# Optimization experiments

Measured on AMD Instinct MI355X. Metric: run time of the kernel, lower is better.

Reference implementation:

```python
import jax, jax.numpy as jnp
import numpy as np

V, E, H, ENC = 10000, 512, 512, 2048
B, T, P = 64, 64, 196


def setup_inputs() -> dict:
    key = jax.random.key(0)
    ks = jax.random.split(key, 12)
    s = 0.02
    return {
        "encoder_out": jax.random.normal(ks[0], (B, P, ENC), jnp.float32),
        "targets": jax.random.randint(ks[1], (B, T), 0, V),
        "embedding": jax.random.normal(ks[2], (V, E), jnp.float32) * s,
        "W_ih": jax.random.normal(ks[3], (4 * H, E), jnp.float32) * s,
        "W_hh": jax.random.normal(ks[4], (4 * H, H), jnp.float32) * s,
        "b_ih": jnp.zeros((4 * H,), jnp.float32),
        "b_hh": jnp.zeros((4 * H,), jnp.float32),
        "Wh": jax.random.normal(ks[5], (H, ENC), jnp.float32) * s,
        "bh": jnp.zeros((H,), jnp.float32),
        "Wc": jax.random.normal(ks[6], (H, ENC), jnp.float32) * s,
        "bc": jnp.zeros((H,), jnp.float32),
        "Wout": jax.random.normal(ks[7], (V, H), jnp.float32) * s,
        "bout": jnp.zeros((V,), jnp.float32),
    }


def reference(encoder_out, targets, embedding, W_ih, W_hh, b_ih, b_hh, Wh, bh, Wc, bc, Wout, bout):
    # init hidden state from mean-pooled encoder features
    mean_enc = encoder_out.mean(axis=1)                      # [B, ENC]
    h0 = jnp.tanh(mean_enc @ Wh.T + bh)                      # [B, H]
    c0 = jnp.tanh(mean_enc @ Wc.T + bc)                      # [B, H]

    Bsz, Tlen = targets.shape
    # teacher forcing (ratio=1.0): input at step t is targets[:, t-1]
    emb = embedding[targets[:, :-1]]                         # [B, T-1, E]
    # precompute input-dependent gate pre-activations (dropout = eval identity)
    xg = jnp.einsum('bte,ge->btg', emb, W_ih) + b_ih + b_hh  # [B, T-1, 4H]

    def step(carry, x):
        h, c = carry
        gates = x + h @ W_hh.T                               # [B, 4H]
        i, f, g, o = jnp.split(gates, 4, axis=-1)
        i = jax.nn.sigmoid(i)
        f = jax.nn.sigmoid(f)
        g = jnp.tanh(g)
        o = jax.nn.sigmoid(o)
        c = f * c + i * g
        h = o * jnp.tanh(c)
        out = h @ Wout.T + bout                              # [B, V]
        return (h, c), out

    _, outs = jax.lax.scan(step, (h0, c0), jnp.swapaxes(xg, 0, 1))
    outs = jnp.swapaxes(outs, 0, 1)                          # [B, T-1, V]
    zeros0 = jnp.zeros((Bsz, 1, outs.shape[-1]), outs.dtype)  # step 0 untouched
    return jnp.concatenate([zeros0, outs], axis=1)           # [B, T, V]
```

## Files before the change

### kernel.cpp

```cpp
#include <hip/hip_runtime.h>

typedef __bf16 bf16x8 __attribute__((ext_vector_type(8)));
typedef float f32x4 __attribute__((ext_vector_type(4)));

static __device__ __forceinline__ unsigned short f2bf(float f) {
    unsigned u = __builtin_bit_cast(unsigned, f);
    unsigned r = u + 0x7fffu + ((u >> 16) & 1u);
    return (unsigned short)(r >> 16);
}

#define GLD_LDS16(g, l) __builtin_amdgcn_global_load_lds( \
    (const __attribute__((address_space(1))) unsigned int*)(const void*)(g), \
    (__attribute__((address_space(3))) unsigned int*)(void*)(l), 16, 0, 0)

__global__ __launch_bounds__(256) void k_prep(
    const float* Wih, const float* Whh, const float* Wh, const float* Wc,
    const float* Wout, const float* emb, const int* targets,
    unsigned short* Wih_b, unsigned short* Whh_b, unsigned short* Wh_b,
    unsigned short* Wc_b, unsigned short* Wout_b, unsigned short* Aemb,
    float* out, int* ctrs, float* ps)
{
    const long N0 = 1048576, N1 = 1048576, N2 = 1048576, N3 = 1048576;
    const long N4 = 5120000, N5 = 2064384, N6 = 640000, N7 = 256, N8 = 65536;
    const long total = N0 + N1 + N2 + N3 + N4 + N5 + N6 + N7 + N8;
    const long stride = (long)gridDim.x * blockDim.x;
    for (long i = (long)blockIdx.x * blockDim.x + threadIdx.x; i < total; i += stride) {
        long j = i;
        if (j < N0) { Wih_b[j] = f2bf(Wih[j]); continue; } j -= N0;
        if (j < N1) { Whh_b[j] = f2bf(Whh[j]); continue; } j -= N1;
        if (j < N2) { Wh_b[j]  = f2bf(Wh[j]);  continue; } j -= N2;
        if (j < N3) { Wc_b[j]  = f2bf(Wc[j]);  continue; } j -= N3;
        if (j < N4) { Wout_b[j] = f2bf(Wout[j]); continue; } j -= N4;
        if (j < N5) {
            long m = j >> 9; int k = (int)(j & 511);
            int b = (int)(m / 63), t = (int)(m - (long)b * 63);
            int row = targets[b * 64 + t];
            Aemb[j] = f2bf(emb[(long)row * 512 + k]);
            continue;
        } j -= N5;
        if (j < N6) {
            long b = j / 10000, v = j - b * 10000;
            out[b * 640000 + v] = 0.f;
            continue;
        } j -= N6;
        if (j < N7) { ctrs[j] = 0; continue; } j -= N7;
        ps[j] = 0.f;
    }
}

__global__ __launch_bounds__(128) void k_mean(const float* enc, unsigned short* mean_b)
{
    int b = blockIdx.y;
    int c = blockIdx.x * 128 + threadIdx.x;
    const float* base = enc + (long)b * 196 * 2048 + c;
    float s0 = 0.f, s1 = 0.f, s2 = 0.f, s3 = 0.f;
    for (int p = 0; p < 196; p += 4) {
        s0 += base[(long)(p + 0) * 2048];
        s1 += base[(long)(p + 1) * 2048];
        s2 += base[(long)(p + 2) * 2048];
        s3 += base[(long)(p + 3) * 2048];
    }
    mean_b[(long)b * 2048 + c] = f2bf((s0 + s1 + s2 + s3) * (1.f / 196.f));
}

__global__ __launch_bounds__(256) void k_h0c0(
    const unsigned short* A, const unsigned short* Whb, const unsigned short* Wcb,
    float* ps)
{
    __shared__ unsigned short As[64 * 40];
    __shared__ unsigned short Bs[64 * 40];
    const int tid = threadIdx.x;
    const int n0 = blockIdx.x * 64;
    const int kc = blockIdx.y * 16;
    const int w = tid >> 6, lane = tid & 63, quad = lane >> 4, l16 = lane & 15;
    const int r = tid >> 2, seg = tid & 3;
    f32x4 acc[4];
#pragma unroll
    for (int i = 0; i < 4; i++) acc[i] = (f32x4){0.f, 0.f, 0.f, 0.f};

    for (int kb = kc; kb < kc + 16; kb++) {
        int k0 = kb * 32;
        *(uint4*)&As[r * 40 + seg * 8] = *(const uint4*)&A[(long)r * 2048 + k0 + seg * 8];
        int ngr = n0 + r;
        const unsigned short* bsrc = (ngr < 512) ? (Whb + (long)ngr * 2048)
                                                 : (Wcb + (long)(ngr - 512) * 2048);
        *(uint4*)&Bs[r * 40 + seg * 8] = *(const uint4*)&bsrc[k0 + seg * 8];
        __syncthreads();
        bf16x8 bfr = *(const bf16x8*)&Bs[(16 * w + l16) * 40 + quad * 8];
#pragma unroll
        for (int mt = 0; mt < 4; mt++) {
            bf16x8 af = *(const bf16x8*)&As[(mt * 16 + l16) * 40 + quad * 8];
            acc[mt] = __builtin_amdgcn_mfma_f32_16x16x32_bf16(af, bfr, acc[mt], 0, 0, 0);
        }
        __syncthreads();
    }
    int ng = n0 + 16 * w + l16;
#pragma unroll
    for (int mt = 0; mt < 4; mt++) {
#pragma unroll
        for (int rr = 0; rr < 4; rr++) {
            int m = mt * 16 + quad * 4 + rr;
            atomicAdd(&ps[(long)m * 1024 + ng], acc[mt][rr]);
        }
    }
}

__global__ __launch_bounds__(256) void k_fin(
    const float* ps, const float* bh, const float* bc,
    unsigned short* Hbuf, float* c0buf)
{
    int i = blockIdx.x * 256 + threadIdx.x;
    int m = i >> 10, ng = i & 1023;
    int j = ng & 511;
    float bias = (ng < 512) ? bh[j] : bc[j];
    float v = tanhf(ps[i] + bias);
    if (ng < 512) Hbuf[(long)m * 512 + j] = f2bf(v);
    else          c0buf[(long)m * 512 + j] = v;
}

__global__ __launch_bounds__(256) void k_xg(
    const unsigned short* A, const unsigned short* Bw,
    const float* bih, const float* bhh, float* xg)
{
    __shared__ unsigned short As[64 * 40];
    __shared__ unsigned short Bs[64 * 40];
    const int tid = threadIdx.x;
    const int n0 = blockIdx.x * 64, m0 = blockIdx.y * 64;
    const int w = tid >> 6, lane = tid & 63, quad = lane >> 4, l16 = lane & 15;
    const int r = tid >> 2, seg = tid & 3;
    f32x4 acc[4];
#pragma unroll
    for (int i = 0; i < 4; i++) acc[i] = (f32x4){0.f, 0.f, 0.f, 0.f};

    for (int kb = 0; kb < 16; kb++) {
        int k0 = kb * 32;
        *(uint4*)&As[r * 40 + seg * 8] = *(const uint4*)&A[(long)(m0 + r) * 512 + k0 + seg * 8];
        *(uint4*)&Bs[r * 40 + seg * 8] = *(const uint4*)&Bw[(long)(n0 + r) * 512 + k0 + seg * 8];
        __syncthreads();
        bf16x8 bfr = *(const bf16x8*)&Bs[(16 * w + l16) * 40 + quad * 8];
#pragma unroll
        for (int mt = 0; mt < 4; mt++) {
            bf16x8 af = *(const bf16x8*)&As[(mt * 16 + l16) * 40 + quad * 8];
            acc[mt] = __builtin_amdgcn_mfma_f32_16x16x32_bf16(af, bfr, acc[mt], 0, 0, 0);
        }
        __syncthreads();
    }
    int ng = n0 + 16 * w + l16;
    float bias = bih[ng] + bhh[ng];
#pragma unroll
    for (int mt = 0; mt < 4; mt++) {
#pragma unroll
        for (int rr = 0; rr < 4; rr++) {
            int m = m0 + mt * 16 + quad * 4 + rr;
            xg[(long)m * 2048 + ng] = acc[mt][rr] + bias;
        }
    }
}

__global__ __launch_bounds__(256, 1) void k_scan(
    const unsigned short* Whh_b, const float* xg, const float* c0buf,
    unsigned short* Hbuf, int* ctrs)
{
    __shared__ unsigned short Wlds[128 * 520];
    __shared__ unsigned short hs[16 * 520];
    __shared__ float gs[16 * 133];
    const int tid = threadIdx.x;
    const int gid = blockIdx.x;
    const int b0 = (gid & 3) * 16;
    const int j0 = (gid >> 2) * 32;
    const int w = tid >> 6, lane = tid & 63, quad = lane >> 4, l16 = lane & 15;
    const int m = tid >> 4, u0 = (tid & 15) * 2;

    for (int nrel = w; nrel < 128; nrel += 4) {
        int q = nrel >> 5, u = nrel & 31;
        *(uint4*)&Wlds[nrel * 520 + lane * 8] =
            *(const uint4*)&Whh_b[(long)(q * 512 + j0 + u) * 512 + lane * 8];
    }
    float2 cr = *(const float2*)&c0buf[(long)(b0 + m) * 512 + j0 + u0];
    float c0v = cr.x, c1v = cr.y;
    int* ctr = ctrs + (gid & 3) * 64;
    __syncthreads();

    for (int s = 1; s < 64; s++) {
        const float* xb = xg + ((long)(b0 + m) * 63 + (s - 1)) * 2048 + j0 + u0;
        float2 xv0 = *(const float2*)(xb + 0);
        float2 xv1 = *(const float2*)(xb + 512);
        float2 xv2 = *(const float2*)(xb + 1024);
        float2 xv3 = *(const float2*)(xb + 1536);

        const unsigned* hsrc = (const unsigned*)(Hbuf + ((long)(s - 1) * 64 + b0) * 512);
        unsigned hv[16];
#pragma unroll
        for (int j = 0; j < 16; j++)
            hv[j] = __hip_atomic_load(hsrc + j * 256 + tid, __ATOMIC_RELAXED,
                                      __HIP_MEMORY_SCOPE_AGENT);
#pragma unroll
        for (int j = 0; j < 16; j++)
            *(unsigned*)&hs[j * 520 + tid * 2] = hv[j];
        __syncthreads();

        f32x4 acc0 = (f32x4){0.f, 0.f, 0.f, 0.f};
        f32x4 acc1 = (f32x4){0.f, 0.f, 0.f, 0.f};
#pragma unroll
        for (int kk = 0; kk < 16; kk++) {
            bf16x8 a  = *(const bf16x8*)&hs[l16 * 520 + kk * 32 + quad * 8];
            bf16x8 bA = *(const bf16x8*)&Wlds[(32 * w + l16) * 520 + kk * 32 + quad * 8];
            bf16x8 bB = *(const bf16x8*)&Wlds[(32 * w + 16 + l16) * 520 + kk * 32 + quad * 8];
            acc0 = __builtin_amdgcn_mfma_f32_16x16x32_bf16(a, bA, acc0, 0, 0, 0);
            acc1 = __builtin_amdgcn_mfma_f32_16x16x32_bf16(a, bB, acc1, 0, 0, 0);
        }
#pragma unroll
        for (int rr = 0; rr < 4; rr++) {
            gs[(quad * 4 + rr) * 133 + 32 * w + l16] = acc0[rr];
            gs[(quad * 4 + rr) * 133 + 32 * w + 16 + l16] = acc1[rr];
        }
        __syncthreads();

        float gi0 = gs[m * 133 + u0]          + xv0.x;
        float gi1 = gs[m * 133 + u0 + 1]      + xv0.y;
        float gf0 = gs[m * 133 + 32 + u0]     + xv1.x;
        float gf1 = gs[m * 133 + 33 + u0]     + xv1.y;
        float gg0 = gs[m * 133 + 64 + u0]     + xv2.x;
        float gg1 = gs[m * 133 + 65 + u0]     + xv2.y;
        float go0 = gs[m * 133 + 96 + u0]     + xv3.x;
        float go1 = gs[m * 133 + 97 + u0]     + xv3.y;
        float cn0 = (1.f / (1.f + __expf(-gf0))) * c0v + (1.f / (1.f + __expf(-gi0))) * tanhf(gg0);
        float cn1 = (1.f / (1.f + __expf(-gf1))) * c1v + (1.f / (1.f + __expf(-gi1))) * tanhf(gg1);
        c0v = cn0; c1v = cn1;
        float h0v = (1.f / (1.f + __expf(-go0))) * tanhf(cn0);
        float h1v = (1.f / (1.f + __expf(-go1))) * tanhf(cn1);
        unsigned hp = (unsigned)f2bf(h0v) | ((unsigned)f2bf(h1v) << 16);
        __hip_atomic_store((unsigned*)(Hbuf + ((long)s * 64 + b0 + m) * 512 + j0 + u0), hp,
                           __ATOMIC_RELAXED, __HIP_MEMORY_SCOPE_AGENT);

        if (s < 63) {
            __syncthreads();
            if (tid == 0) {
                __hip_atomic_fetch_add(ctr, 1, __ATOMIC_RELEASE, __HIP_MEMORY_SCOPE_AGENT);
                int target = s * 16;
                while (__hip_atomic_load(ctr, __ATOMIC_RELAXED, __HIP_MEMORY_SCOPE_AGENT) < target) {}
            }
            __syncthreads();
        }
    }
}

__global__ __launch_bounds__(256) void k_out(
    const unsigned short* A, const unsigned short* Wob, const float* bout, float* out)
{
    __shared__ unsigned short As[128 * 32];
    __shared__ unsigned short Bs[128 * 32];
    const int tid = threadIdx.x;
    const int n0 = blockIdx.x * 128, m0 = blockIdx.y * 128;
    const int w = tid >> 6, lane = tid & 63, quad = lane >> 4, l16 = lane & 15;
    const int wm = w >> 1, wn = w & 1;
    const int gr = lane >> 2, gc = (lane & 3) * 8;

    f32x4 acc[4][4];
#pragma unroll
    for (int i = 0; i < 4; i++)
#pragma unroll
        for (int j = 0; j < 4; j++) acc[i][j] = (f32x4){0.f, 0.f, 0.f, 0.f};

    for (int kb = 0; kb < 16; kb++) {
        int k0 = kb * 32;
#pragma unroll
        for (int p = 0; p < 2; p++) {
            int rowa = m0 + p * 64 + w * 16 + gr;
            GLD_LDS16(A + (long)rowa * 512 + k0 + gc, As + (p * 64 + w * 16) * 32);
            int rowb = n0 + p * 64 + w * 16 + gr;
            GLD_LDS16(Wob + (long)rowb * 512 + k0 + gc, Bs + (p * 64 + w * 16) * 32);
        }
        __syncthreads();
        bf16x8 af[4], bf[4];
#pragma unroll
        for (int mt = 0; mt < 4; mt++)
            af[mt] = *(const bf16x8*)&As[(wm * 64 + mt * 16 + l16) * 32 + quad * 8];
#pragma unroll
        for (int nt = 0; nt < 4; nt++)
            bf[nt] = *(const bf16x8*)&Bs[(wn * 64 + nt * 16 + l16) * 32 + quad * 8];
#pragma unroll
        for (int mt = 0; mt < 4; mt++)
#pragma unroll
            for (int nt = 0; nt < 4; nt++)
                acc[mt][nt] = __builtin_amdgcn_mfma_f32_16x16x32_bf16(af[mt], bf[nt], acc[mt][nt], 0, 0, 0);
        __syncthreads();
    }
#pragma unroll
    for (int nt = 0; nt < 4; nt++) {
        int n = n0 + wn * 64 + nt * 16 + l16;
        if (n >= 10000) continue;
        float bias = bout[n];
#pragma unroll
        for (int mt = 0; mt < 4; mt++) {
#pragma unroll
            for (int rr = 0; rr < 4; rr++) {
                int r = m0 + wm * 64 + mt * 16 + quad * 4 + rr;
                if (r < 4032) {
                    int s = (r >> 6) + 1, b = r & 63;
                    out[((long)b * 64 + s) * 10000 + n] = acc[mt][nt][rr] + bias;
                }
            }
        }
    }
}

extern "C" void kernel_launch(void* const* d_in, const int* in_sizes, int n_in,
                              void* d_out, int out_size, void* d_ws, size_t ws_size,
                              hipStream_t stream)
{
    const float* enc     = (const float*)d_in[0];
    const int*   targets = (const int*)d_in[1];
    const float* emb     = (const float*)d_in[2];
    const float* Wih     = (const float*)d_in[3];
    const float* Whh     = (const float*)d_in[4];
    const float* bih     = (const float*)d_in[5];
    const float* bhh     = (const float*)d_in[6];
    const float* Wh      = (const float*)d_in[7];
    const float* bh      = (const float*)d_in[8];
    const float* Wc      = (const float*)d_in[9];
    const float* bc      = (const float*)d_in[10];
    const float* Wout    = (const float*)d_in[11];
    const float* bout    = (const float*)d_in[12];
    float* out = (float*)d_out;

    char* ws = (char*)d_ws;
    size_t off = 0;
    auto alloc = [&](size_t bytes) {
        void* p = ws + off;
        off = (off + bytes + 255) & ~(size_t)255;
        return p;
    };
    unsigned short* mean_b = (unsigned short*)alloc((size_t)64 * 2048 * 2);
    unsigned short* Wih_b  = (unsigned short*)alloc((size_t)2048 * 512 * 2);
    unsigned short* Whh_b  = (unsigned short*)alloc((size_t)2048 * 512 * 2);
    unsigned short* Wh_b   = (unsigned short*)alloc((size_t)512 * 2048 * 2);
    unsigned short* Wc_b   = (unsigned short*)alloc((size_t)512 * 2048 * 2);
    unsigned short* Wout_b = (unsigned short*)alloc((size_t)10000 * 512 * 2);
    unsigned short* Aemb   = (unsigned short*)alloc((size_t)4032 * 512 * 2);
    float*          xg     = (float*)alloc((size_t)4032 * 2048 * 4);
    unsigned short* Hbuf   = (unsigned short*)alloc((size_t)64 * 64 * 512 * 2);
    float*          c0buf  = (float*)alloc((size_t)64 * 512 * 4);
    int*            ctrs   = (int*)alloc(256 * 4);
    float*          ps     = (float*)alloc((size_t)64 * 1024 * 4);

    k_prep<<<4096, 256, 0, stream>>>(Wih, Whh, Wh, Wc, Wout, emb, targets,
                                     Wih_b, Whh_b, Wh_b, Wc_b, Wout_b, Aemb, out, ctrs, ps);
    k_mean<<<dim3(16, 64), 128, 0, stream>>>(enc, mean_b);
    k_h0c0<<<dim3(16, 4), 256, 0, stream>>>(mean_b, Wh_b, Wc_b, ps);
    k_fin<<<256, 256, 0, stream>>>(ps, bh, bc, Hbuf, c0buf);
    k_xg<<<dim3(32, 63), 256, 0, stream>>>(Aemb, Wih_b, bih, bhh, xg);
    k_scan<<<64, 256, 0, stream>>>(Whh_b, xg, c0buf, Hbuf, ctrs);
    k_out<<<dim3(79, 32), 256, 0, stream>>>(Hbuf + 64 * 512, Wout_b, bout, out);
}
```

Baseline: 653.3 us.

## Vectorize prep, fold mean into prep, merge h0c0 and xg GEMMs, swizzle k_out tiles

The prep kernel is rewritten with block-range dispatch and 8-wide vectorized fp32-to-bf16 conversion, and it now also computes the encoder mean, which removes the separate k_mean launch. The h0/c0 GEMM and the xg GEMM are merged into one launch. The xg part switches to 128x128 tiles loaded with direct global-to-LDS loads, with buffers padded to cover the partial last tile. k_out now uses a 1D grid with a tile remapping meant to improve L2 reuse. Together these aim to cut launch overhead and memory inefficiency in the pre-scan stages, at the cost of more branchy dispatch code.

```diff
diff --git a/kernel.cpp b/kernel.cpp
--- a/kernel.cpp
+++ b/kernel.cpp
@@ -15,92 +15,176 @@
 
 __global__ __launch_bounds__(256) void k_prep(
     const float* Wih, const float* Whh, const float* Wh, const float* Wc,
-    const float* Wout, const float* emb, const int* targets,
+    const float* Wout, const float* emb, const int* targets, const float* enc,
     unsigned short* Wih_b, unsigned short* Whh_b, unsigned short* Wh_b,
     unsigned short* Wc_b, unsigned short* Wout_b, unsigned short* Aemb,
-    float* out, int* ctrs, float* ps)
-{
-    const long N0 = 1048576, N1 = 1048576, N2 = 1048576, N3 = 1048576;
-    const long N4 = 5120000, N5 = 2064384, N6 = 640000, N7 = 256, N8 = 65536;
-    const long total = N0 + N1 + N2 + N3 + N4 + N5 + N6 + N7 + N8;
-    const long stride = (long)gridDim.x * blockDim.x;
-    for (long i = (long)blockIdx.x * blockDim.x + threadIdx.x; i < total; i += stride) {
-        long j = i;
-        if (j < N0) { Wih_b[j] = f2bf(Wih[j]); continue; } j -= N0;
-        if (j < N1) { Whh_b[j] = f2bf(Whh[j]); continue; } j -= N1;
-        if (j < N2) { Wh_b[j]  = f2bf(Wh[j]);  continue; } j -= N2;
-        if (j < N3) { Wc_b[j]  = f2bf(Wc[j]);  continue; } j -= N3;
-        if (j < N4) { Wout_b[j] = f2bf(Wout[j]); continue; } j -= N4;
-        if (j < N5) {
-            long m = j >> 9; int k = (int)(j & 511);
-            int b = (int)(m / 63), t = (int)(m - (long)b * 63);
-            int row = targets[b * 64 + t];
-            Aemb[j] = f2bf(emb[(long)row * 512 + k]);
-            continue;
-        } j -= N5;
-        if (j < N6) {
-            long b = j / 10000, v = j - b * 10000;
-            out[b * 640000 + v] = 0.f;
-            continue;
-        } j -= N6;
-        if (j < N7) { ctrs[j] = 0; continue; } j -= N7;
-        ps[j] = 0.f;
-    }
-}
-
-__global__ __launch_bounds__(128) void k_mean(const float* enc, unsigned short* mean_b)
-{
-    int b = blockIdx.y;
-    int c = blockIdx.x * 128 + threadIdx.x;
-    const float* base = enc + (long)b * 196 * 2048 + c;
-    float s0 = 0.f, s1 = 0.f, s2 = 0.f, s3 = 0.f;
-    for (int p = 0; p < 196; p += 4) {
-        s0 += base[(long)(p + 0) * 2048];
-        s1 += base[(long)(p + 1) * 2048];
-        s2 += base[(long)(p + 2) * 2048];
-        s3 += base[(long)(p + 3) * 2048];
-    }
-    mean_b[(long)b * 2048 + c] = f2bf((s0 + s1 + s2 + s3) * (1.f / 196.f));
-}
-
-__global__ __launch_bounds__(256) void k_h0c0(
-    const unsigned short* A, const unsigned short* Whb, const unsigned short* Wcb,
-    float* ps)
-{
-    __shared__ unsigned short As[64 * 40];
-    __shared__ unsigned short Bs[64 * 40];
-    const int tid = threadIdx.x;
-    const int n0 = blockIdx.x * 64;
-    const int kc = blockIdx.y * 16;
+    float* out, int* ctrs, float* ps, unsigned short* mean_b)
+{
+    const int bid = blockIdx.x, tid = threadIdx.x;
+
+    if (bid < 2048) {
+        long f = ((long)bid * 256 + tid) * 8;
+        int a = (int)(f >> 20);
+        long off = f & 1048575;
+        const float* s = (a == 0) ? Wih : (a == 1) ? Whh : (a == 2) ? Wh : Wc;
+        unsigned short* d = (a == 0) ? Wih_b : (a == 1) ? Whh_b : (a == 2) ? Wh_b : Wc_b;
+        float4 v0 = *(const float4*)(s + off);
+        float4 v1 = *(const float4*)(s + off + 4);
+        unsigned short r[8] = {f2bf(v0.x), f2bf(v0.y), f2bf(v0.z), f2bf(v0.w),
+                               f2bf(v1.x), f2bf(v1.y), f2bf(v1.z), f2bf(v1.w)};
+        *(uint4*)(d + off) = *(uint4*)r;
+        return;
+    }
+    if (bid < 4548) {
+        long f = ((long)(bid - 2048) * 256 + tid) * 8;
+        float4 v0 = *(const float4*)(Wout + f);
+        float4 v1 = *(const float4*)(Wout + f + 4);
+        unsigned short r[8] = {f2bf(v0.x), f2bf(v0.y), f2bf(v0.z), f2bf(v0.w),
+                               f2bf(v1.x), f2bf(v1.y), f2bf(v1.z), f2bf(v1.w)};
+        *(uint4*)(Wout_b + f) = *(uint4*)r;
+        return;
+    }
+    if (bid < 5556) {
+        unsigned t = (unsigned)(bid - 4548) * 256 + tid;
+        unsigned row = t >> 6;
+        unsigned col = (t & 63) * 8;
+        unsigned b = row / 63u, tt = row - b * 63u;
+        int trg = targets[b * 64 + tt];
+        const float* s = emb + (long)trg * 512 + col;
+        float4 v0 = *(const float4*)(s);
+        float4 v1 = *(const float4*)(s + 4);
+        unsigned short r[8] = {f2bf(v0.x), f2bf(v0.y), f2bf(v0.z), f2bf(v0.w),
+                               f2bf(v1.x), f2bf(v1.y), f2bf(v1.z), f2bf(v1.w)};
+        *(uint4*)(Aemb + (long)row * 512 + col) = *(uint4*)r;
+        return;
+    }
+    if (bid < 6181) {
+        unsigned idx = ((unsigned)(bid - 5556) * 256 + tid) * 4;
+        unsigned b = idx / 10000u, v = idx - b * 10000u;
+        *(float4*)(out + (long)b * 640000 + v) = (float4){0.f, 0.f, 0.f, 0.f};
+        return;
+    }
+    if (bid < 6246) {
+        int rel = bid - 6181;
+        if (rel < 64) {
+            unsigned idx = ((unsigned)rel * 256 + tid) * 4;
+            *(float4*)(ps + idx) = (float4){0.f, 0.f, 0.f, 0.f};
+        } else {
+            ctrs[tid] = 0;
+        }
+        return;
+    }
+    {
+        unsigned idx = (unsigned)(bid - 6246) * 256 + tid;
+        unsigned b = idx >> 11, c = idx & 2047;
+        const float* base = enc + (long)b * 196 * 2048 + c;
+        float s0 = 0.f, s1 = 0.f, s2 = 0.f, s3 = 0.f;
+        for (int p = 0; p < 196; p += 4) {
+            s0 += base[(long)(p + 0) * 2048];
+            s1 += base[(long)(p + 1) * 2048];
+            s2 += base[(long)(p + 2) * 2048];
+            s3 += base[(long)(p + 3) * 2048];
+        }
+        mean_b[(long)b * 2048 + c] = f2bf((s0 + s1 + s2 + s3) * (1.f / 196.f));
+    }
+}
+
+__global__ __launch_bounds__(256) void k_gemm2(
+    const unsigned short* mean_b, const unsigned short* Whb, const unsigned short* Wcb,
+    float* ps,
+    const unsigned short* Aemb, const unsigned short* Wihb,
+    const float* bih, const float* bhh, float* xg)
+{
+    __shared__ __align__(16) char smem[16384];
+    const int bid = blockIdx.x, tid = threadIdx.x;
     const int w = tid >> 6, lane = tid & 63, quad = lane >> 4, l16 = lane & 15;
-    const int r = tid >> 2, seg = tid & 3;
-    f32x4 acc[4];
-#pragma unroll
-    for (int i = 0; i < 4; i++) acc[i] = (f32x4){0.f, 0.f, 0.f, 0.f};
-
-    for (int kb = kc; kb < kc + 16; kb++) {
+
+    if (bid < 64) {
+        unsigned short* As = (unsigned short*)smem;
+        unsigned short* Bs = (unsigned short*)(smem + 5120);
+        const int n0 = (bid & 15) * 64;
+        const int kc = (bid >> 4) * 16;
+        const int r = tid >> 2, seg = tid & 3;
+        f32x4 acc[4];
+#pragma unroll
+        for (int i = 0; i < 4; i++) acc[i] = (f32x4){0.f, 0.f, 0.f, 0.f};
+
+        for (int kb = kc; kb < kc + 16; kb++) {
+            int k0 = kb * 32;
+            *(uint4*)&As[r * 40 + seg * 8] = *(const uint4*)&mean_b[(long)r * 2048 + k0 + seg * 8];
+            int ngr = n0 + r;
+            const unsigned short* bsrc = (ngr < 512) ? (Whb + (long)ngr * 2048)
+                                                     : (Wcb + (long)(ngr - 512) * 2048);
+            *(uint4*)&Bs[r * 40 + seg * 8] = *(const uint4*)&bsrc[k0 + seg * 8];
+            __syncthreads();
+            bf16x8 bfr = *(const bf16x8*)&Bs[(16 * w + l16) * 40 + quad * 8];
+#pragma unroll
+            for (int mt = 0; mt < 4; mt++) {
+                bf16x8 af = *(const bf16x8*)&As[(mt * 16 + l16) * 40 + quad * 8];
+                acc[mt] = __builtin_amdgcn_mfma_f32_16x16x32_bf16(af, bfr, acc[mt], 0, 0, 0);
+            }
+            __syncthreads();
+        }
+        int ng = n0 + 16 * w + l16;
+#pragma unroll
+        for (int mt = 0; mt < 4; mt++) {
+#pragma unroll
+            for (int rr = 0; rr < 4; rr++) {
+                int m = mt * 16 + quad * 4 + rr;
+                atomicAdd(&ps[(long)m * 1024 + ng], acc[mt][rr]);
+            }
+        }
+        return;
+    }
+
+    unsigned short* As = (unsigned short*)smem;
+    unsigned short* Bs = (unsigned short*)(smem + 8192);
+    const int rel = bid - 64;
+    const int n0 = (rel & 15) * 128, m0 = (rel >> 4) * 128;
+    const int wm = w >> 1, wn = w & 1;
+    const int gr = lane >> 2, gc = (lane & 3) * 8;
+
+    f32x4 acc[4][4];
+#pragma unroll
+    for (int i = 0; i < 4; i++)
+#pragma unroll
+        for (int j = 0; j < 4; j++) acc[i][j] = (f32x4){0.f, 0.f, 0.f, 0.f};
+
+    for (int kb = 0; kb < 16; kb++) {
         int k0 = kb * 32;
-        *(uint4*)&As[r * 40 + seg * 8] = *(const uint4*)&A[(long)r * 2048 + k0 + seg * 8];
-        int ngr = n0 + r;
-        const unsigned short* bsrc = (ngr < 512) ? (Whb + (long)ngr * 2048)
-                                                 : (Wcb + (long)(ngr - 512) * 2048);
-        *(uint4*)&Bs[r * 40 + seg * 8] = *(const uint4*)&bsrc[k0 + seg * 8];
-        __syncthreads();
-        bf16x8 bfr = *(const bf16x8*)&Bs[(16 * w + l16) * 40 + quad * 8];
+#pragma unroll
+        for (int p = 0; p < 2; p++) {
+            int rowa = m0 + p * 64 + w * 16 + gr;
+            GLD_LDS16(Aemb + (long)rowa * 512 + k0 + gc, As + (p * 64 + w * 16) * 32);
+            int rowb = n0 + p * 64 + w * 16 + gr;
+            GLD_LDS16(Wihb + (long)rowb * 512 + k0 + gc, Bs + (p * 64 + w * 16) * 32);
+        }
+        __syncthreads();
+        bf16x8 af[4], bf[4];
+#pragma unroll
+        for (int mt = 0; mt < 4; mt++)
+            af[mt] = *(const bf16x8*)&As[(wm * 64 + mt * 16 + l16) * 32 + quad * 8];
+#pragma unroll
+        for (int nt = 0; nt < 4; nt++)
+            bf[nt] = *(const bf16x8*)&Bs[(wn * 64 + nt * 16 + l16) * 32 + quad * 8];
+#pragma unroll
+        for (int mt = 0; mt < 4; mt++)
+#pragma unroll
+            for (int nt = 0; nt < 4; nt++)
+                acc[mt][nt] = __builtin_amdgcn_mfma_f32_16x16x32_bf16(af[mt], bf[nt], acc[mt][nt], 0, 0, 0);
+        __syncthreads();
+    }
+#pragma unroll
+    for (int nt = 0; nt < 4; nt++) {
+        int n = n0 + wn * 64 + nt * 16 + l16;
+        float bias = bih[n] + bhh[n];
 #pragma unroll
         for (int mt = 0; mt < 4; mt++) {
-            bf16x8 af = *(const bf16x8*)&As[(mt * 16 + l16) * 40 + quad * 8];
-            acc[mt] = __builtin_amdgcn_mfma_f32_16x16x32_bf16(af, bfr, acc[mt], 0, 0, 0);
-        }
-        __syncthreads();
-    }
-    int ng = n0 + 16 * w + l16;
-#pragma unroll
-    for (int mt = 0; mt < 4; mt++) {
-#pragma unroll
-        for (int rr = 0; rr < 4; rr++) {
-            int m = mt * 16 + quad * 4 + rr;
-            atomicAdd(&ps[(long)m * 1024 + ng], acc[mt][rr]);
+#pragma unroll
+            for (int rr = 0; rr < 4; rr++) {
+                int r = m0 + wm * 64 + mt * 16 + quad * 4 + rr;
+                if (r < 4032) xg[(long)r * 2048 + n] = acc[mt][nt][rr] + bias;
+            }
         }
     }
 }
@@ -116,45 +200,6 @@
     float v = tanhf(ps[i] + bias);
     if (ng < 512) Hbuf[(long)m * 512 + j] = f2bf(v);
     else          c0buf[(long)m * 512 + j] = v;
-}
-
-__global__ __launch_bounds__(256) void k_xg(
-    const unsigned short* A, const unsigned short* Bw,
-    const float* bih, const float* bhh, float* xg)
-{
-    __shared__ unsigned short As[64 * 40];
-    __shared__ unsigned short Bs[64 * 40];
-    const int tid = threadIdx.x;
-    const int n0 = blockIdx.x * 64, m0 = blockIdx.y * 64;
-    const int w = tid >> 6, lane = tid & 63, quad = lane >> 4, l16 = lane & 15;
-    const int r = tid >> 2, seg = tid & 3;
-    f32x4 acc[4];
-#pragma unroll
-    for (int i = 0; i < 4; i++) acc[i] = (f32x4){0.f, 0.f, 0.f, 0.f};
-
-    for (int kb = 0; kb < 16; kb++) {
-        int k0 = kb * 32;
-        *(uint4*)&As[r * 40 + seg * 8] = *(const uint4*)&A[(long)(m0 + r) * 512 + k0 + seg * 8];
-        *(uint4*)&Bs[r * 40 + seg * 8] = *(const uint4*)&Bw[(long)(n0 + r) * 512 + k0 + seg * 8];
-        __syncthreads();
-        bf16x8 bfr = *(const bf16x8*)&Bs[(16 * w + l16) * 40 + quad * 8];
-#pragma unroll
-        for (int mt = 0; mt < 4; mt++) {
-            bf16x8 af = *(const bf16x8*)&As[(mt * 16 + l16) * 40 + quad * 8];
-            acc[mt] = __builtin_amdgcn_mfma_f32_16x16x32_bf16(af, bfr, acc[mt], 0, 0, 0);
-        }
-        __syncthreads();
-    }
-    int ng = n0 + 16 * w + l16;
-    float bias = bih[ng] + bhh[ng];
-#pragma unroll
-    for (int mt = 0; mt < 4; mt++) {
-#pragma unroll
-        for (int rr = 0; rr < 4; rr++) {
-            int m = m0 + mt * 16 + quad * 4 + rr;
-            xg[(long)m * 2048 + ng] = acc[mt][rr] + bias;
-        }
-    }
 }
 
 __global__ __launch_bounds__(256, 1) void k_scan(
@@ -251,7 +296,8 @@
     __shared__ unsigned short As[128 * 32];
     __shared__ unsigned short Bs[128 * 32];
     const int tid = threadIdx.x;
-    const int n0 = blockIdx.x * 128, m0 = blockIdx.y * 128;
+    const int tile = (blockIdx.x & 7) * 316 + (blockIdx.x >> 3);
+    const int n0 = (tile >> 5) * 128, m0 = (tile & 31) * 128;
     const int w = tid >> 6, lane = tid & 63, quad = lane >> 4, l16 = lane & 15;
     const int wm = w >> 1, wn = w & 1;
     const int gr = lane >> 2, gc = (lane & 3) * 8;
@@ -337,19 +383,19 @@
     unsigned short* Wh_b   = (unsigned short*)alloc((size_t)512 * 2048 * 2);
     unsigned short* Wc_b   = (unsigned short*)alloc((size_t)512 * 2048 * 2);
     unsigned short* Wout_b = (unsigned short*)alloc((size_t)10000 * 512 * 2);
-    unsigned short* Aemb   = (unsigned short*)alloc((size_t)4032 * 512 * 2);
+    unsigned short* Aemb   = (unsigned short*)alloc((size_t)(4032 + 64) * 512 * 2);
     float*          xg     = (float*)alloc((size_t)4032 * 2048 * 4);
-    unsigned short* Hbuf   = (unsigned short*)alloc((size_t)64 * 64 * 512 * 2);
+    unsigned short* Hbuf   = (unsigned short*)alloc((size_t)(64 * 64 + 64) * 512 * 2);
     float*          c0buf  = (float*)alloc((size_t)64 * 512 * 4);
     int*            ctrs   = (int*)alloc(256 * 4);
     float*          ps     = (float*)alloc((size_t)64 * 1024 * 4);
 
-    k_prep<<<4096, 256, 0, stream>>>(Wih, Whh, Wh, Wc, Wout, emb, targets,
-                                     Wih_b, Whh_b, Wh_b, Wc_b, Wout_b, Aemb, out, ctrs, ps);
-    k_mean<<<dim3(16, 64), 128, 0, stream>>>(enc, mean_b);
-    k_h0c0<<<dim3(16, 4), 256, 0, stream>>>(mean_b, Wh_b, Wc_b, ps);
+    k_prep<<<6758, 256, 0, stream>>>(Wih, Whh, Wh, Wc, Wout, emb, targets, enc,
+                                     Wih_b, Whh_b, Wh_b, Wc_b, Wout_b, Aemb,
+                                     out, ctrs, ps, mean_b);
+    k_gemm2<<<576, 256, 0, stream>>>(mean_b, Wh_b, Wc_b, ps,
+                                     Aemb, Wih_b, bih, bhh, xg);
     k_fin<<<256, 256, 0, stream>>>(ps, bh, bc, Hbuf, c0buf);
-    k_xg<<<dim3(32, 63), 256, 0, stream>>>(Aemb, Wih_b, bih, bhh, xg);
     k_scan<<<64, 256, 0, stream>>>(Whh_b, xg, c0buf, Hbuf, ctrs);
-    k_out<<<dim3(79, 32), 256, 0, stream>>>(Hbuf + 64 * 512, Wout_b, bout, out);
-}
+    k_out<<<2528, 256, 0, stream>>>(Hbuf + 64 * 512, Wout_b, bout, out);
+}
```

After: 627.4 us. 1.04x faster.
